# Kernel optimization log

Measured on AMD Instinct MI355X. Metric: run time of the kernel, lower is better.

Reference implementation:

```python
import jax, jax.numpy as jnp
import numpy as np

B, S, D = 64, 2048, 64

def setup_inputs() -> dict:
    key = jax.random.key(0)
    kq, kk, kv = jax.random.split(key, 3)
    queries = jax.random.normal(kq, (B, S, D), dtype=jnp.float32)
    keys = jax.random.normal(kk, (B, S, D), dtype=jnp.float32)
    values = jax.random.normal(kv, (B, S, D), dtype=jnp.float32)
    return {"queries": queries, "keys": keys, "values": values}

def reference(queries, keys, values):
    # scores: [B, Sq, Sk] = Q @ K^T / sqrt(d)
    d = queries.shape[-1]
    scale = 1.0 / jnp.sqrt(jnp.asarray(d, dtype=queries.dtype))
    scores = jnp.einsum('bqd,bkd->bqk', queries, keys) * scale
    attn = jax.nn.softmax(scores, axis=-1)
    # dropout is identity in eval/reference mode
    return jnp.einsum('bqk,bkd->bqd', attn, values)
```

## Files before the change

kernel.cpp:

```cpp
#include <hip/hip_runtime.h>


typedef short bf16x8 __attribute__((ext_vector_type(8)));
typedef float f32x16 __attribute__((ext_vector_type(16)));

#define SQK 0.18033688011112042f

__device__ __forceinline__ short f2bf(float x) {
  unsigned u = __float_as_uint(x);
  u = (u + 0x7fffu + ((u >> 16) & 1u)) >> 16;
  return (short)u;
}

__device__ __forceinline__ unsigned pk2(float lo, float hi) {
  unsigned r;
  asm("v_cvt_pk_bf16_f32 %0, %1, %2" : "=v"(r) : "v"(lo), "v"(hi));
  return r;
}

__global__ __launch_bounds__(512) void DotProductAttention_44573170598739_kernel(
    const float* __restrict__ Q, const float* __restrict__ K,
    const float* __restrict__ V, float* __restrict__ O) {
  constexpr int S = 2048, D = 64;
  const int b   = blockIdx.x;
  const int q0  = blockIdx.y * 256;
  const int tid = threadIdx.x;
  const int w    = tid >> 6;
  const int lane = tid & 63;
  const int hi   = lane >> 5;
  const int r32  = lane & 31;

  __shared__ __align__(16) short ksh[64 * 72];
  __shared__ __align__(16) short vsh[64 * 72];

  bf16x8 qf[4];
#pragma unroll
  for (int dd = 0; dd < 4; ++dd) {
    const float* qp = Q + ((size_t)b * S + q0 + w * 32 + r32) * D + dd * 16 + hi * 8;
    float4 x = ((const float4*)qp)[0];
    float4 y = ((const float4*)qp)[1];
    bf16x8 f;
    f[0] = f2bf(x.x * SQK); f[1] = f2bf(x.y * SQK);
    f[2] = f2bf(x.z * SQK); f[3] = f2bf(x.w * SQK);
    f[4] = f2bf(y.x * SQK); f[5] = f2bf(y.y * SQK);
    f[6] = f2bf(y.z * SQK); f[7] = f2bf(y.w * SQK);
    qf[dd] = f;
  }

  f32x16 oacc[2] = {};
  float rs = 0.f;
  const f32x16 z16 = {};

  const float* Kb = K + (size_t)b * S * D;
  const float* Vb = V + (size_t)b * S * D;

  float4 kx[2];
  float  vv[8];
#pragma unroll
  for (int i = 0; i < 2; ++i)
    kx[i] = ((const float4*)Kb)[tid + 512 * i];
#pragma unroll
  for (int j = 0; j < 8; ++j)
    vv[j] = Vb[(w * 8 + j) * D + lane];

  const int vcb = 16 * (w >> 1) + 4 * (w & 1);

  for (int kt = 0; kt < S; kt += 64) {
#pragma unroll
    for (int i = 0; i < 2; ++i) {
      int f = 4 * tid + 2048 * i;
      int row = f >> 6, col = f & 63;
      uint2 pk = { pk2(kx[i].x, kx[i].y), pk2(kx[i].z, kx[i].w) };
      *(uint2*)&ksh[row * 72 + col] = pk;
    }
    {
      uint2 plo = { pk2(vv[0], vv[1]), pk2(vv[2], vv[3]) };
      uint2 phi = { pk2(vv[4], vv[5]), pk2(vv[6], vv[7]) };
      *(uint2*)&vsh[lane * 72 + vcb]     = plo;
      *(uint2*)&vsh[lane * 72 + vcb + 8] = phi;
    }
    __syncthreads();

#pragma unroll
    for (int t = 0; t < 2; ++t) {
      bf16x8 kf[4];
#pragma unroll
      for (int dd = 0; dd < 4; ++dd)
        kf[dd] = *(const bf16x8*)&ksh[(t * 32 + r32) * 72 + dd * 16 + hi * 8];

      if (t == 0) {
        const int kt2 = (kt + 64 < S) ? kt + 64 : 0;
        const float* Kg2 = Kb + (size_t)kt2 * D;
        const float* Vg2 = Vb + (size_t)kt2 * D;
#pragma unroll
        for (int i = 0; i < 2; ++i)
          kx[i] = ((const float4*)Kg2)[tid + 512 * i];
#pragma unroll
        for (int j = 0; j < 8; ++j)
          vv[j] = Vg2[(w * 8 + j) * D + lane];
      }

      f32x16 z = __builtin_amdgcn_mfma_f32_32x32x16_bf16(kf[0], qf[0], z16, 0, 0, 0);
      z = __builtin_amdgcn_mfma_f32_32x32x16_bf16(kf[1], qf[1], z, 0, 0, 0);
      z = __builtin_amdgcn_mfma_f32_32x32x16_bf16(kf[2], qf[2], z, 0, 0, 0);
      z = __builtin_amdgcn_mfma_f32_32x32x16_bf16(kf[3], qf[3], z, 0, 0, 0);

#pragma unroll
      for (int h = 0; h < 2; ++h) {
        float e0 = __builtin_amdgcn_exp2f(z[8 * h + 0]);
        float e1 = __builtin_amdgcn_exp2f(z[8 * h + 1]);
        float e2 = __builtin_amdgcn_exp2f(z[8 * h + 2]);
        float e3 = __builtin_amdgcn_exp2f(z[8 * h + 3]);
        float e4 = __builtin_amdgcn_exp2f(z[8 * h + 4]);
        float e5 = __builtin_amdgcn_exp2f(z[8 * h + 5]);
        float e6 = __builtin_amdgcn_exp2f(z[8 * h + 6]);
        float e7 = __builtin_amdgcn_exp2f(z[8 * h + 7]);
        rs += ((e0 + e1) + (e2 + e3)) + ((e4 + e5) + (e6 + e7));
        union { bf16x8 v; unsigned u[4]; } pu;
        pu.u[0] = pk2(e0, e1); pu.u[1] = pk2(e2, e3);
        pu.u[2] = pk2(e4, e5); pu.u[3] = pk2(e6, e7);

        const int cb = t * 32 + h * 16 + hi * 8;
        bf16x8 vf0 = *(const bf16x8*)&vsh[(r32) * 72 + cb];
        bf16x8 vf1 = *(const bf16x8*)&vsh[(32 + r32) * 72 + cb];

        oacc[0] = __builtin_amdgcn_mfma_f32_32x32x16_bf16(pu.v, vf0, oacc[0], 0, 0, 0);
        oacc[1] = __builtin_amdgcn_mfma_f32_32x32x16_bf16(pu.v, vf1, oacc[1], 0, 0, 0);
      }
    }
    __syncthreads();
  }

  float tot = rs + __shfl_xor(rs, 32);
#pragma unroll
  for (int g = 0; g < 16; ++g) {
    int rq = (g & 3) + 8 * (g >> 2) + 4 * hi;
    float inv = 1.0f / __shfl(tot, rq);
    int q = q0 + w * 32 + rq;
    float* op = O + ((size_t)b * S + q) * D + r32;
    op[0]  = oacc[0][g] * inv;
    op[32] = oacc[1][g] * inv;
  }
}

extern "C" void kernel_launch(void* const* d_in, const int* in_sizes, int n_in,
                              void* d_out, int out_size, void* d_ws, size_t ws_size,
                              hipStream_t stream) {
  (void)in_sizes; (void)n_in; (void)out_size; (void)d_ws; (void)ws_size;
  const float* Q = (const float*)d_in[0];
  const float* K = (const float*)d_in[1];
  const float* V = (const float*)d_in[2];
  float* O = (float*)d_out;
  dim3 grid(64, 2048 / 256, 1);
  dim3 block(512, 1, 1);
  hipLaunchKernelGGL(DotProductAttention_44573170598739_kernel,
                     grid, block, 0, stream, Q, K, V, O);
}
```

Baseline: 202.4 us.

## Double-buffer K/V shared tiles and raise priority around MFMA blocks

Splits the K/V LDS tiles into two buffers so the next tile is converted and stored while the current one is consumed. This removes one of the two block barriers per iteration. Wraps the MFMA groups in s_setprio to favour matrix issue across waves. It also adds a launch-bounds occupancy hint of 4, which may limit registers, and doubles LDS use per block.

```diff
diff --git a/kernel.cpp b/kernel.cpp
--- a/kernel.cpp
+++ b/kernel.cpp
@@ -18,7 +18,7 @@
   return r;
 }
 
-__global__ __launch_bounds__(512) void DotProductAttention_44573170598739_kernel(
+__global__ __launch_bounds__(512, 4) void DotProductAttention_44573170598739_kernel(
     const float* __restrict__ Q, const float* __restrict__ K,
     const float* __restrict__ V, float* __restrict__ O) {
   constexpr int S = 2048, D = 64;
@@ -30,8 +30,8 @@
   const int hi   = lane >> 5;
   const int r32  = lane & 31;
 
-  __shared__ __align__(16) short ksh[64 * 72];
-  __shared__ __align__(16) short vsh[64 * 72];
+  __shared__ __align__(16) short ksh[2][64 * 72];
+  __shared__ __align__(16) short vsh[2][64 * 72];
 
   bf16x8 qf[4];
 #pragma unroll
@@ -54,44 +54,57 @@
   const float* Kb = K + (size_t)b * S * D;
   const float* Vb = V + (size_t)b * S * D;
 
+  const int vcb = 16 * (w >> 1) + 4 * (w & 1);
+
   float4 kx[2];
   float  vv[8];
+
 #pragma unroll
   for (int i = 0; i < 2; ++i)
     kx[i] = ((const float4*)Kb)[tid + 512 * i];
 #pragma unroll
   for (int j = 0; j < 8; ++j)
     vv[j] = Vb[(w * 8 + j) * D + lane];
+#pragma unroll
+  for (int i = 0; i < 2; ++i) {
+    int f = 4 * tid + 2048 * i;
+    int row = f >> 6, col = f & 63;
+    uint2 pk = { pk2(kx[i].x, kx[i].y), pk2(kx[i].z, kx[i].w) };
+    *(uint2*)&ksh[0][row * 72 + col] = pk;
+  }
+  {
+    uint2 plo = { pk2(vv[0], vv[1]), pk2(vv[2], vv[3]) };
+    uint2 phi = { pk2(vv[4], vv[5]), pk2(vv[6], vv[7]) };
+    *(uint2*)&vsh[0][lane * 72 + vcb]     = plo;
+    *(uint2*)&vsh[0][lane * 72 + vcb + 8] = phi;
+  }
+#pragma unroll
+  for (int i = 0; i < 2; ++i)
+    kx[i] = ((const float4*)(Kb + 64 * D))[tid + 512 * i];
+#pragma unroll
+  for (int j = 0; j < 8; ++j)
+    vv[j] = Vb[(64 + w * 8 + j) * D + lane];
+  __syncthreads();
 
-  const int vcb = 16 * (w >> 1) + 4 * (w & 1);
-
-  for (int kt = 0; kt < S; kt += 64) {
+  int p = 0;
+  for (int kt = 0; kt < S; kt += 64, p ^= 1) {
+    if (kt + 64 < S) {
 #pragma unroll
-    for (int i = 0; i < 2; ++i) {
-      int f = 4 * tid + 2048 * i;
-      int row = f >> 6, col = f & 63;
-      uint2 pk = { pk2(kx[i].x, kx[i].y), pk2(kx[i].z, kx[i].w) };
-      *(uint2*)&ksh[row * 72 + col] = pk;
-    }
-    {
-      uint2 plo = { pk2(vv[0], vv[1]), pk2(vv[2], vv[3]) };
-      uint2 phi = { pk2(vv[4], vv[5]), pk2(vv[6], vv[7]) };
-      *(uint2*)&vsh[lane * 72 + vcb]     = plo;
-      *(uint2*)&vsh[lane * 72 + vcb + 8] = phi;
-    }
-    __syncthreads();
-
-#pragma unroll
-    for (int t = 0; t < 2; ++t) {
-      bf16x8 kf[4];
-#pragma unroll
-      for (int dd = 0; dd < 4; ++dd)
-        kf[dd] = *(const bf16x8*)&ksh[(t * 32 + r32) * 72 + dd * 16 + hi * 8];
-
-      if (t == 0) {
-        const int kt2 = (kt + 64 < S) ? kt + 64 : 0;
-        const float* Kg2 = Kb + (size_t)kt2 * D;
-        const float* Vg2 = Vb + (size_t)kt2 * D;
+      for (int i = 0; i < 2; ++i) {
+        int f = 4 * tid + 2048 * i;
+        int row = f >> 6, col = f & 63;
+        uint2 pk = { pk2(kx[i].x, kx[i].y), pk2(kx[i].z, kx[i].w) };
+        *(uint2*)&ksh[p ^ 1][row * 72 + col] = pk;
+      }
+      {
+        uint2 plo = { pk2(vv[0], vv[1]), pk2(vv[2], vv[3]) };
+        uint2 phi = { pk2(vv[4], vv[5]), pk2(vv[6], vv[7]) };
+        *(uint2*)&vsh[p ^ 1][lane * 72 + vcb]     = plo;
+        *(uint2*)&vsh[p ^ 1][lane * 72 + vcb + 8] = phi;
+      }
+      if (kt + 128 < S) {
+        const float* Kg2 = Kb + (size_t)(kt + 128) * D;
+        const float* Vg2 = Vb + (size_t)(kt + 128) * D;
 #pragma unroll
         for (int i = 0; i < 2; ++i)
           kx[i] = ((const float4*)Kg2)[tid + 512 * i];
@@ -99,11 +112,23 @@
         for (int j = 0; j < 8; ++j)
           vv[j] = Vg2[(w * 8 + j) * D + lane];
       }
+    }
 
+    const short* kshp = ksh[p];
+    const short* vshp = vsh[p];
+#pragma unroll
+    for (int t = 0; t < 2; ++t) {
+      bf16x8 kf[4];
+#pragma unroll
+      for (int dd = 0; dd < 4; ++dd)
+        kf[dd] = *(const bf16x8*)&kshp[(t * 32 + r32) * 72 + dd * 16 + hi * 8];
+
+      __builtin_amdgcn_s_setprio(1);
       f32x16 z = __builtin_amdgcn_mfma_f32_32x32x16_bf16(kf[0], qf[0], z16, 0, 0, 0);
       z = __builtin_amdgcn_mfma_f32_32x32x16_bf16(kf[1], qf[1], z, 0, 0, 0);
       z = __builtin_amdgcn_mfma_f32_32x32x16_bf16(kf[2], qf[2], z, 0, 0, 0);
       z = __builtin_amdgcn_mfma_f32_32x32x16_bf16(kf[3], qf[3], z, 0, 0, 0);
+      __builtin_amdgcn_s_setprio(0);
 
 #pragma unroll
       for (int h = 0; h < 2; ++h) {
@@ -121,11 +146,13 @@
         pu.u[2] = pk2(e4, e5); pu.u[3] = pk2(e6, e7);
 
         const int cb = t * 32 + h * 16 + hi * 8;
-        bf16x8 vf0 = *(const bf16x8*)&vsh[(r32) * 72 + cb];
-        bf16x8 vf1 = *(const bf16x8*)&vsh[(32 + r32) * 72 + cb];
+        bf16x8 vf0 = *(const bf16x8*)&vshp[r32 * 72 + cb];
+        bf16x8 vf1 = *(const bf16x8*)&vshp[(32 + r32) * 72 + cb];
 
+        __builtin_amdgcn_s_setprio(1);
         oacc[0] = __builtin_amdgcn_mfma_f32_32x32x16_bf16(pu.v, vf0, oacc[0], 0, 0, 0);
         oacc[1] = __builtin_amdgcn_mfma_f32_32x32x16_bf16(pu.v, vf1, oacc[1], 0, 0, 0);
+        __builtin_amdgcn_s_setprio(0);
       }
     }
     __syncthreads();
```

Result: faster. 190.7 us (-5.8%).
